# Performance work log

Hardware: AMD Instinct MI355X
Metric: run time of the kernel (lower is better)

## Reference

```python
import jax, jax.numpy as jnp
import numpy as np

N_NODES = 50000
BN_EPS = 1e-5


def gcn_conv(x, W, b, src, dst):
    # PyG GCNConv: linear, add self-loops, symmetric degree normalization, scatter-add, bias.
    h = x @ W                                        # [N, D]
    n = x.shape[0]
    deg = jax.ops.segment_sum(jnp.ones(src.shape[0], x.dtype), dst,
                              num_segments=n) + 1.0  # +1 for self-loop
    dinv = jnp.where(deg > 0, jax.lax.rsqrt(deg), 0.0)
    norm = dinv[src] * dinv[dst]                     # [E]
    agg = jax.ops.segment_sum(h[src] * norm[:, None], dst, num_segments=n)
    agg = agg + h * (dinv * dinv)[:, None]           # self-loop contribution
    return agg + b


def batch_norm(x, gamma, beta):
    # training-mode BN over the node axis (biased variance, as torch)
    mu = jnp.mean(x, axis=0)
    var = jnp.mean((x - mu) ** 2, axis=0)
    return (x - mu) * jax.lax.rsqrt(var + BN_EPS) * gamma + beta


def setup_inputs() -> dict:
    key = jax.random.key(0)
    ks = jax.random.split(key, 8)
    D, C = 128, 10
    x = jax.random.normal(ks[0], (N_NODES, D), dtype=jnp.float32)
    edge_index = jax.random.randint(ks[1], (2, 640000), 0, N_NODES, dtype=jnp.int32)
    s = 1.0 / np.sqrt(D)
    return {
        "x": x,
        "edge_index": edge_index,
        "W1": jax.random.normal(ks[2], (D, D), dtype=jnp.float32) * s,
        "b1": jnp.zeros((D,), jnp.float32),
        "gamma1": jnp.ones((D,), jnp.float32),
        "beta1": jnp.zeros((D,), jnp.float32),
        "W2": jax.random.normal(ks[3], (D, D), dtype=jnp.float32) * s,
        "b2": jnp.zeros((D,), jnp.float32),
        "gamma2": jnp.ones((D,), jnp.float32),
        "beta2": jnp.zeros((D,), jnp.float32),
        "lin1_w": jax.random.normal(ks[4], (D, D), dtype=jnp.float32) * s,
        "lin1_b": jnp.zeros((D,), jnp.float32),
        "lin2_w": jax.random.normal(ks[5], (D, C), dtype=jnp.float32) * s,
        "lin2_b": jnp.zeros((C,), jnp.float32),
    }


def reference(x, edge_index, W1, b1, gamma1, beta1, W2, b2, gamma2, beta2,
              lin1_w, lin1_b, lin2_w, lin2_b):
    src, dst = edge_index[0], edge_index[1]
    # layer 1: GCNConv -> ReLU -> BN (dropout = identity at eval)
    h = jax.nn.relu(gcn_conv(x, W1, b1, src, dst))
    h = batch_norm(h, gamma1, beta1)
    # layer 2
    h = jax.nn.relu(gcn_conv(h, W2, b2, src, dst))
    h = batch_norm(h, gamma2, beta2)
    # MLP head
    h = jax.nn.relu(h @ lin1_w + lin1_b)
    logits = h @ lin2_w + lin2_b
    return jax.nn.log_softmax(logits, axis=-1)
```

## Files before the change

### kernel.cpp

```cpp
#include <hip/hip_runtime.h>
#include <hip/hip_bf16.h>
#include <math.h>

typedef unsigned int uint;
typedef unsigned short ushort;
using f32x4 = __attribute__((ext_vector_type(4))) float;
using s16x8 = __attribute__((ext_vector_type(8))) short;

#define NSLOT 64

__device__ __forceinline__ float bflo(uint u) { return __uint_as_float(u << 16); }
__device__ __forceinline__ float bfhi(uint u) { return __uint_as_float(u & 0xffff0000u); }
__device__ __forceinline__ ushort f2bf(float f) {
    uint u = __float_as_uint(f);
    return (ushort)((u + 0x7fffu + ((u >> 16) & 1u)) >> 16);
}
__device__ __forceinline__ float sel4f(float a, float b, float c, float d, int i) {
    float r = a; r = (i == 1) ? b : r; r = (i == 2) ? c : r; r = (i == 3) ? d : r; return r;
}
__device__ __forceinline__ int sel4i(int a, int b, int c, int d, int i) {
    int r = a; r = (i == 1) ? b : r; r = (i == 2) ? c : r; r = (i == 3) ? d : r; return r;
}


__global__ void deg_count(const int* __restrict__ dst, int* __restrict__ deg, int E) {
    int e = blockIdx.x * 256 + threadIdx.x;
    if (e < E) atomicAdd(&deg[dst[e]], 1);
}

__global__ __launch_bounds__(256) void deg_block_sum(const int* __restrict__ deg,
                                                     int* __restrict__ bsum, int N) {
    __shared__ int s[256];
    int i = blockIdx.x * 256 + threadIdx.x;
    s[threadIdx.x] = (i < N) ? deg[i] : 0;
    __syncthreads();
    #pragma unroll
    for (int off = 128; off > 0; off >>= 1) {
        if (threadIdx.x < off) s[threadIdx.x] += s[threadIdx.x + off];
        __syncthreads();
    }
    if (threadIdx.x == 0) bsum[blockIdx.x] = s[0];
}

__global__ __launch_bounds__(256) void fill_rowstart(const int* __restrict__ deg,
                                                     const int* __restrict__ bsum,
                                                     int* __restrict__ row_start,
                                                     int* __restrict__ cursor,
                                                     float* __restrict__ dinv,
                                                     int N, int E, int nblk) {
    __shared__ int s[256];
    __shared__ int sb[256];
    int t = threadIdx.x;
    int i = blockIdx.x * 256 + t;
    int dg = (i < N) ? deg[i] : 0;
    s[t] = dg;
    sb[t] = (t < nblk) ? bsum[t] : 0;
    __syncthreads();
    for (int off = 1; off < 256; off <<= 1) {
        int v1 = (t >= off) ? s[t - off] : 0;
        int v2 = (t >= off) ? sb[t - off] : 0;
        __syncthreads();
        s[t] += v1;
        sb[t] += v2;
        __syncthreads();
    }
    if (i < N) {
        int boff = (blockIdx.x == 0) ? 0 : sb[blockIdx.x - 1];
        int excl = boff + s[t] - dg;
        row_start[i] = excl;
        cursor[i] = excl;
        dinv[i] = rsqrtf((float)dg + 1.0f);
    }
    if (i == 0) row_start[N] = E;
}

__global__ void csr_fill(const int* __restrict__ src, const int* __restrict__ dst,
                         const float* __restrict__ dinv, int* __restrict__ cursor,
                         int2* __restrict__ csr2, int E) {
    int e = blockIdx.x * 256 + threadIdx.x;
    if (e >= E) return;
    int s = src[e], d = dst[e];
    int pos = atomicAdd(&cursor[d], 1);
    csr2[pos] = make_int2(s, __float_as_int(dinv[s] * dinv[d]));
}


__global__ __launch_bounds__(256) void prep_weights(const float* __restrict__ W1,
                                                    const float* __restrict__ W2,
                                                    const float* __restrict__ W3,
                                                    const float* __restrict__ l2w,
                                                    const float* __restrict__ l2b,
                                                    ushort* __restrict__ wt1,
                                                    ushort* __restrict__ wt2,
                                                    ushort* __restrict__ wt3,
                                                    ushort* __restrict__ w2bf,
                                                    float* __restrict__ b2pad) {
    int i = blockIdx.x * 256 + threadIdx.x;
    int li = i & 16383;
    int k = li >> 7, n = li & 127;
    const float* Ws = (i < 16384) ? W1 : (i < 32768) ? W2 : W3;
    ushort* Wd = (i < 16384) ? wt1 : (i < 32768) ? wt2 : wt3;
    Wd[n * 128 + k] = f2bf(Ws[li]);
    if (i < 2048) {
        int c = i >> 7, kk = i & 127;
        float v = (c < 10) ? l2w[kk * 10 + c] : 0.f;
        w2bf[c * 128 + kk] = f2bf(v);
    }
    if (i < 16) b2pad[i] = (i < 10) ? l2b[i] : -1e30f;
}


template<bool XF32, bool AFF, bool BIAS, bool RELU, bool HEAD>
__global__ __launch_bounds__(256) void gemm_mfma(const void* __restrict__ Xv,
                                                 const float* __restrict__ scale,
                                                 const float* __restrict__ shift,
                                                 const ushort* __restrict__ Bt,
                                                 const float* __restrict__ bias,
                                                 ushort* __restrict__ Y,
                                                 const ushort* __restrict__ W2bf,
                                                 const float* __restrict__ b2pad,
                                                 float* __restrict__ OUT, int N) {
    __shared__ char smem[16384 + 32768];
    char* Al = smem;
    char* Bl = smem + 16384;

    int tid = threadIdx.x;
    int brow = blockIdx.x * 64;

    {
        int n = tid >> 1, h = tid & 1;
        const uint4* srcp = (const uint4*)(Bt + n * 128 + h * 64);
        #pragma unroll
        for (int i = 0; i < 8; ++i) {
            uint4 v = srcp[i];
            int u = (h * 8 + i) ^ (n & 7);
            *(uint4*)(Bl + n * 256 + u * 16) = v;
        }
    }
    {
        int r = tid >> 2, c0 = (tid & 3) * 32;
        int row = brow + r;
        bool ok = row < N;
        uint pk[16];
        if (XF32) {
            const float* Xr = (const float*)Xv + (size_t)row * 128 + c0;
            #pragma unroll
            for (int i = 0; i < 16; ++i) {
                float f0 = ok ? Xr[i * 2] : 0.f;
                float f1 = ok ? Xr[i * 2 + 1] : 0.f;
                pk[i] = (uint)f2bf(f0) | ((uint)f2bf(f1) << 16);
            }
        } else {
            const uint* Xr = (const uint*)((const ushort*)Xv + (size_t)row * 128 + c0);
            #pragma unroll
            for (int i = 0; i < 16; ++i) {
                uint u = ok ? Xr[i] : 0u;
                float f0 = bflo(u), f1 = bfhi(u);
                if (AFF) {
                    int c = c0 + i * 2;
                    f0 = f0 * scale[c] + shift[c];
                    f1 = f1 * scale[c + 1] + shift[c + 1];
                }
                pk[i] = (uint)f2bf(f0) | ((uint)f2bf(f1) << 16);
            }
        }
        #pragma unroll
        for (int i = 0; i < 4; ++i) {
            int u = ((tid & 3) * 4 + i) ^ (r & 7);
            *(uint4*)(Al + r * 256 + u * 16) = *(uint4*)&pk[i * 4];
        }
    }
    __syncthreads();

    int lane = tid & 63, w = tid >> 6;
    int m = lane & 15, g = lane >> 4;
    int wr = w * 16;

    f32x4 acc[8];
    #pragma unroll
    for (int nt = 0; nt < 8; ++nt) acc[nt] = (f32x4){0.f, 0.f, 0.f, 0.f};

    #pragma unroll
    for (int kk = 0; kk < 4; ++kk) {
        int u = (kk * 4 + g) ^ (m & 7);
        s16x8 a = *(const s16x8*)(Al + (wr + m) * 256 + u * 16);
        #pragma unroll
        for (int nt = 0; nt < 8; ++nt) {
            s16x8 b = *(const s16x8*)(Bl + (nt * 16 + m) * 256 + u * 16);
            acc[nt] = __builtin_amdgcn_mfma_f32_16x16x32_bf16(a, b, acc[nt], 0, 0, 0);
        }
    }

    float bv[8];
    if (BIAS) {
        #pragma unroll
        for (int nt = 0; nt < 8; ++nt) bv[nt] = bias[nt * 16 + m];
    }

    if (!HEAD) {
        #pragma unroll
        for (int i = 0; i < 4; ++i) {
            int row = brow + wr + g * 4 + i;
            if (row < N) {
                #pragma unroll
                for (int nt = 0; nt < 8; ++nt) {
                    float v = acc[nt][i];
                    if (BIAS) v += bv[nt];
                    if (RELU) v = fmaxf(v, 0.f);
                    Y[(size_t)row * 128 + nt * 16 + m] = f2bf(v);
                }
            }
        }
    } else {
        #pragma unroll
        for (int i = 0; i < 4; ++i) {
            int r = wr + g * 4 + i;
            #pragma unroll
            for (int nt = 0; nt < 8; ++nt) {
                float v = acc[nt][i] + bv[nt];
                v = fmaxf(v, 0.f);
                int col = nt * 16 + m;
                int u = (col >> 3) ^ (r & 7);
                *(ushort*)(Al + r * 256 + u * 16 + (col & 7) * 2) = f2bf(v);
            }
        }
        __syncthreads();
        float b2v = b2pad[m];
        f32x4 lg = (f32x4){b2v, b2v, b2v, b2v};
        #pragma unroll
        for (int kk = 0; kk < 4; ++kk) {
            int u = (kk * 4 + g) ^ (m & 7);
            s16x8 a = *(const s16x8*)(Al + (wr + m) * 256 + u * 16);
            s16x8 b = *(const s16x8*)(&W2bf[m * 128 + (kk * 4 + g) * 8]);
            lg = __builtin_amdgcn_mfma_f32_16x16x32_bf16(a, b, lg, 0, 0, 0);
        }
        #pragma unroll
        for (int i = 0; i < 4; ++i) {
            float v = lg[i];
            float mx = v;
            #pragma unroll
            for (int off = 8; off > 0; off >>= 1) mx = fmaxf(mx, __shfl_xor(mx, off, 64));
            float ex = expf(v - mx);
            float sm = ex;
            #pragma unroll
            for (int off = 8; off > 0; off >>= 1) sm += __shfl_xor(sm, off, 64);
            float res = v - (mx + logf(sm));
            int grow = brow + wr + g * 4 + i;
            if (m < 10 && grow < N) OUT[(size_t)grow * 10 + m] = res;
        }
    }
}


__global__ __launch_bounds__(256) void gather_fused(const ushort* __restrict__ H,
                                                    const int* __restrict__ row_start,
                                                    const int2* __restrict__ csr2,
                                                    const float* __restrict__ dinv,
                                                    const float* __restrict__ bias,
                                                    ushort* __restrict__ Y,
                                                    float* __restrict__ bnpart, int N) {
    int g = threadIdx.x >> 6, lane = threadIdx.x & 63;
    int d = lane * 2;
    float b0 = bias[d], b1 = bias[d + 1];
    float s0 = 0.f, s1 = 0.f, ss0 = 0.f, ss1 = 0.f;

    int nchunks = (N + 3) / 4;
    int chunk = blockIdx.x * 4 + g;

    if (chunk < nchunks) {
        int c = chunk * 4;
        int nn = min(4, N - c);

        int rsv = row_start[c + min(lane, nn)];
        int rs0 = __shfl(rsv, 0);
        int rs1 = __shfl(rsv, min(1, nn));
        int rs2 = __shfl(rsv, min(2, nn));
        int rs3 = __shfl(rsv, min(3, nn));
        int rs4 = __shfl(rsv, nn);

        float dvv = dinv[c + min(lane, nn - 1)];
        float dv0 = __shfl(dvv, 0);
        float dv1 = __shfl(dvv, min(1, nn - 1));
        float dv2 = __shfl(dvv, min(2, nn - 1));
        float dv3 = __shfl(dvv, min(3, nn - 1));

        uint h0 = *(const uint*)&H[(size_t)c * 128 + d];
        uint h1 = (nn > 1) ? *(const uint*)&H[(size_t)(c + 1) * 128 + d] : 0u;
        uint h2 = (nn > 2) ? *(const uint*)&H[(size_t)(c + 2) * 128 + d] : 0u;
        uint h3 = (nn > 3) ? *(const uint*)&H[(size_t)(c + 3) * 128 + d] : 0u;

        float i0_0 = bflo(h0) * dv0 * dv0 + b0, i1_0 = bfhi(h0) * dv0 * dv0 + b1;
        float i0_1 = bflo(h1) * dv1 * dv1 + b0, i1_1 = bfhi(h1) * dv1 * dv1 + b1;
        float i0_2 = bflo(h2) * dv2 * dv2 + b0, i1_2 = bfhi(h2) * dv2 * dv2 + b1;
        float i0_3 = bflo(h3) * dv3 * dv3 + b0, i1_3 = bfhi(h3) * dv3 * dv3 + b1;

        int e0 = rs0, eend = rs4;
        int seg = 0;
        int nextb = rs1;
        float a0 = i0_0, a1 = i1_0;

        for (int base = e0; base < eend; base += 64) {
            int cnt = min(64, eend - base);
            int2 me = (lane < cnt) ? csr2[base + lane] : make_int2(0, 0);
            int sl = me.x;
            float nl = __int_as_float(me.y);

            for (int j = 0; j < cnt; j += 16) {
                int mm = min(16, cnt - j);
                uint v[16]; float nr[16];
                #pragma unroll
                for (int k = 0; k < 16; ++k) {
                    int idx = min(j + k, cnt - 1);
                    int sk = __shfl(sl, idx);
                    float nk = __shfl(nl, idx);
                    nr[k] = (k < mm) ? nk : 0.f;
                    v[k] = *(const uint*)&H[(size_t)sk * 128 + d];
                }
                #pragma unroll
                for (int k = 0; k < 16; ++k) {
                    if (k < mm) {
                        int e = base + j + k;
                        while (e >= nextb) {
                            float r0 = fmaxf(a0, 0.f), r1 = fmaxf(a1, 0.f);
                            *(uint*)&Y[(size_t)(c + seg) * 128 + d] =
                                (uint)f2bf(r0) | ((uint)f2bf(r1) << 16);
                            s0 += r0; ss0 += r0 * r0; s1 += r1; ss1 += r1 * r1;
                            seg++;
                            a0 = sel4f(i0_0, i0_1, i0_2, i0_3, seg);
                            a1 = sel4f(i1_0, i1_1, i1_2, i1_3, seg);
                            nextb = sel4i(rs1, rs2, rs3, rs4, seg);
                        }
                        a0 += bflo(v[k]) * nr[k];
                        a1 += bfhi(v[k]) * nr[k];
                    }
                }
            }
        }
        for (;;) {
            float r0 = fmaxf(a0, 0.f), r1 = fmaxf(a1, 0.f);
            *(uint*)&Y[(size_t)(c + seg) * 128 + d] = (uint)f2bf(r0) | ((uint)f2bf(r1) << 16);
            s0 += r0; ss0 += r0 * r0; s1 += r1; ss1 += r1 * r1;
            seg++;
            if (seg >= nn) break;
            a0 = sel4f(i0_0, i0_1, i0_2, i0_3, seg);
            a1 = sel4f(i1_0, i1_1, i1_2, i1_3, seg);
            nextb = sel4i(rs1, rs2, rs3, rs4, seg);
        }
    }

    float* bp = bnpart + (size_t)(blockIdx.x & (NSLOT - 1)) * 256;
    __shared__ float red[4][128];
    red[g][d] = s0; red[g][d + 1] = s1;
    __syncthreads();
    if (g == 0) {
        atomicAdd(&bp[d],     red[0][d] + red[1][d] + red[2][d] + red[3][d]);
        atomicAdd(&bp[d + 1], red[0][d + 1] + red[1][d + 1] + red[2][d + 1] + red[3][d + 1]);
    }
    __syncthreads();
    red[g][d] = ss0; red[g][d + 1] = ss1;
    __syncthreads();
    if (g == 0) {
        atomicAdd(&bp[128 + d],     red[0][d] + red[1][d] + red[2][d] + red[3][d]);
        atomicAdd(&bp[128 + d + 1], red[0][d + 1] + red[1][d + 1] + red[2][d + 1] + red[3][d + 1]);
    }
}

__global__ void bnfinalize(float* __restrict__ bnpart,
                           const float* __restrict__ gamma, const float* __restrict__ beta,
                           float* __restrict__ scale, float* __restrict__ shift, float invN) {
    int d = threadIdx.x;
    float sum = 0.f, ss = 0.f;
    #pragma unroll 8
    for (int s = 0; s < NSLOT; ++s) {
        sum += bnpart[s * 256 + d];
        ss  += bnpart[s * 256 + 128 + d];
        bnpart[s * 256 + d] = 0.f;
        bnpart[s * 256 + 128 + d] = 0.f;
    }
    float mu  = sum * invN;
    float var = ss * invN - mu * mu;
    float sc  = gamma[d] * rsqrtf(var + 1e-5f);
    scale[d] = sc;
    shift[d] = beta[d] - mu * sc;
}


static inline char* align16(char* p) { return (char*)(((uintptr_t)p + 15) & ~(uintptr_t)15); }

extern "C" void kernel_launch(void* const* d_in, const int* in_sizes, int n_in,
                              void* d_out, int out_size, void* d_ws, size_t ws_size,
                              hipStream_t stream) {
    const float* x    = (const float*)d_in[0];
    const int*   ei   = (const int*)d_in[1];
    const float* W1   = (const float*)d_in[2];
    const float* b1   = (const float*)d_in[3];
    const float* g1   = (const float*)d_in[4];
    const float* be1  = (const float*)d_in[5];
    const float* W2   = (const float*)d_in[6];
    const float* b2   = (const float*)d_in[7];
    const float* g2   = (const float*)d_in[8];
    const float* be2  = (const float*)d_in[9];
    const float* l1w  = (const float*)d_in[10];
    const float* l1b  = (const float*)d_in[11];
    const float* l2w  = (const float*)d_in[12];
    const float* l2b  = (const float*)d_in[13];
    float* out = (float*)d_out;

    int N = in_sizes[0] / 128;
    int E = in_sizes[1] / 2;
    const int* srcp = ei;
    const int* dstp = ei + E;

    char* w = (char*)d_ws;
    ushort* bufA  = (ushort*)w;  w = align16(w + (size_t)N * 128 * 2);
    ushort* bufB  = (ushort*)w;  w = align16(w + (size_t)N * 128 * 2);
    int*   degc   = (int*)w;     w += (size_t)N * 4;
    float* bnpart = (float*)w;   w = align16(w + (size_t)NSLOT * 256 * 4);
    float* dinv   = (float*)w;   w = align16(w + (size_t)N * 4);
    int*   row_st = (int*)w;     w = align16(w + (size_t)(N + 1) * 4);
    int*   cursor = (int*)w;     w = align16(w + (size_t)N * 4);
    int*   bsum   = (int*)w;     w = align16(w + 256 * 4);
    int2*  csr2   = (int2*)w;    w = align16(w + (size_t)E * 8);
    float* scale  = (float*)w;   w = align16(w + 128 * 4);
    float* shift  = (float*)w;   w = align16(w + 128 * 4);
    ushort* wt1   = (ushort*)w;  w = align16(w + 16384 * 2);
    ushort* wt2   = (ushort*)w;  w = align16(w + 16384 * 2);
    ushort* wt3   = (ushort*)w;  w = align16(w + 16384 * 2);
    ushort* w2bf  = (ushort*)w;  w = align16(w + 2048 * 2);
    float* b2pad  = (float*)w;   w = align16(w + 16 * 4);

    int eg = (E + 255) / 256;
    int ng = (N + 255) / 256;
    int gemm_grid = (N + 63) / 64;
    int nchunks = (N + 3) / 4;
    int gather_grid = (nchunks + 3) / 4;

    hipMemsetAsync(degc, 0, ((size_t)N + NSLOT * 256) * 4, stream);
    deg_count<<<eg, 256, 0, stream>>>(dstp, degc, E);
    deg_block_sum<<<ng, 256, 0, stream>>>(degc, bsum, N);
    fill_rowstart<<<ng, 256, 0, stream>>>(degc, bsum, row_st, cursor, dinv, N, E, ng);
    csr_fill<<<eg, 256, 0, stream>>>(srcp, dstp, dinv, cursor, csr2, E);
    prep_weights<<<192, 256, 0, stream>>>(W1, W2, l1w, l2w, l2b, wt1, wt2, wt3, w2bf, b2pad);

    gemm_mfma<true, false, false, false, false><<<gemm_grid, 256, 0, stream>>>(
        x, nullptr, nullptr, wt1, nullptr, bufA, nullptr, nullptr, nullptr, N);
    gather_fused<<<gather_grid, 256, 0, stream>>>(bufA, row_st, csr2, dinv, b1, bufB, bnpart, N);
    bnfinalize<<<1, 128, 0, stream>>>(bnpart, g1, be1, scale, shift, 1.0f / N);

    gemm_mfma<false, true, false, false, false><<<gemm_grid, 256, 0, stream>>>(
        bufB, scale, shift, wt2, nullptr, bufA, nullptr, nullptr, nullptr, N);
    gather_fused<<<gather_grid, 256, 0, stream>>>(bufA, row_st, csr2, dinv, b2, bufB, bnpart, N);
    bnfinalize<<<1, 128, 0, stream>>>(bnpart, g2, be2, scale, shift, 1.0f / N);

    gemm_mfma<false, true, true, true, true><<<gemm_grid, 256, 0, stream>>>(
        bufB, scale, shift, wt3, l1b, nullptr, w2bf, b2pad, out, N);
}
```

Measured before the change: 329.5 us.

## Factor GCN normalization into GEMM prescale and drop per-edge weights from CSR

The GEMM epilogue now multiplies each output row by dinv[row], so the gather only sums neighbor features and scales by the destination dinv. This lets the CSR store only source indices (4 bytes per edge instead of 8), cutting gather index traffic and per-edge multiplies. The GEMM also processes two 64-row tiles per block to reuse the staged weight tile, and the degree-count and CSR-fill kernels handle two edges per thread. Rounding the prescaled features to bf16 changes numerics slightly, and the doubled shared memory may reduce occupancy.

After: 323.3 us. About the same (-1.9%).

```diff
diff --git a/kernel.cpp b/kernel.cpp
--- a/kernel.cpp
+++ b/kernel.cpp
@@ -24,8 +24,15 @@
 
 
 __global__ void deg_count(const int* __restrict__ dst, int* __restrict__ deg, int E) {
-    int e = blockIdx.x * 256 + threadIdx.x;
-    if (e < E) atomicAdd(&deg[dst[e]], 1);
+    int e0 = blockIdx.x * 512 + threadIdx.x;
+    int e1 = e0 + 256;
+    if (e1 < E) {
+        int dA = dst[e0], dB = dst[e1];
+        atomicAdd(&deg[dA], 1);
+        atomicAdd(&deg[dB], 1);
+    } else if (e0 < E) {
+        atomicAdd(&deg[dst[e0]], 1);
+    }
 }
 
 __global__ __launch_bounds__(256) void deg_block_sum(const int* __restrict__ deg,
@@ -75,13 +82,21 @@
 }
 
 __global__ void csr_fill(const int* __restrict__ src, const int* __restrict__ dst,
-                         const float* __restrict__ dinv, int* __restrict__ cursor,
-                         int2* __restrict__ csr2, int E) {
-    int e = blockIdx.x * 256 + threadIdx.x;
-    if (e >= E) return;
-    int s = src[e], d = dst[e];
-    int pos = atomicAdd(&cursor[d], 1);
-    csr2[pos] = make_int2(s, __float_as_int(dinv[s] * dinv[d]));
+                         int* __restrict__ cursor, int* __restrict__ csr_src, int E) {
+    int e0 = blockIdx.x * 512 + threadIdx.x;
+    int e1 = e0 + 256;
+    if (e1 < E) {
+        int sA = src[e0], dA = dst[e0];
+        int sB = src[e1], dB = dst[e1];
+        int pA = atomicAdd(&cursor[dA], 1);
+        int pB = atomicAdd(&cursor[dB], 1);
+        csr_src[pA] = sA;
+        csr_src[pB] = sB;
+    } else if (e0 < E) {
+        int s = src[e0], d = dst[e0];
+        int p = atomicAdd(&cursor[d], 1);
+        csr_src[p] = s;
+    }
 }
 
 
@@ -110,22 +125,22 @@
 }
 
 
-template<bool XF32, bool AFF, bool BIAS, bool RELU, bool HEAD>
+template<bool XF32, bool AFF, bool PRESCALE, bool HEAD>
 __global__ __launch_bounds__(256) void gemm_mfma(const void* __restrict__ Xv,
                                                  const float* __restrict__ scale,
                                                  const float* __restrict__ shift,
                                                  const ushort* __restrict__ Bt,
                                                  const float* __restrict__ bias,
+                                                 const float* __restrict__ dinv,
                                                  ushort* __restrict__ Y,
                                                  const ushort* __restrict__ W2bf,
                                                  const float* __restrict__ b2pad,
                                                  float* __restrict__ OUT, int N) {
-    __shared__ char smem[16384 + 32768];
-    char* Al = smem;
-    char* Bl = smem + 16384;
+    __shared__ char smem[2 * 16384 + 32768];
+    char* Bl = smem + 32768;
 
     int tid = threadIdx.x;
-    int brow = blockIdx.x * 64;
+    int brow = blockIdx.x * 128;
 
     {
         int n = tid >> 1, h = tid & 1;
@@ -137,116 +152,119 @@
             *(uint4*)(Bl + n * 256 + u * 16) = v;
         }
     }
-    {
-        int r = tid >> 2, c0 = (tid & 3) * 32;
-        int row = brow + r;
-        bool ok = row < N;
-        uint pk[16];
-        if (XF32) {
-            const float* Xr = (const float*)Xv + (size_t)row * 128 + c0;
-            #pragma unroll
-            for (int i = 0; i < 16; ++i) {
-                float f0 = ok ? Xr[i * 2] : 0.f;
-                float f1 = ok ? Xr[i * 2 + 1] : 0.f;
-                pk[i] = (uint)f2bf(f0) | ((uint)f2bf(f1) << 16);
-            }
-        } else {
-            const uint* Xr = (const uint*)((const ushort*)Xv + (size_t)row * 128 + c0);
-            #pragma unroll
-            for (int i = 0; i < 16; ++i) {
-                uint u = ok ? Xr[i] : 0u;
-                float f0 = bflo(u), f1 = bfhi(u);
-                if (AFF) {
-                    int c = c0 + i * 2;
-                    f0 = f0 * scale[c] + shift[c];
-                    f1 = f1 * scale[c + 1] + shift[c + 1];
-                }
-                pk[i] = (uint)f2bf(f0) | ((uint)f2bf(f1) << 16);
-            }
-        }
-        #pragma unroll
-        for (int i = 0; i < 4; ++i) {
-            int u = ((tid & 3) * 4 + i) ^ (r & 7);
-            *(uint4*)(Al + r * 256 + u * 16) = *(uint4*)&pk[i * 4];
-        }
-    }
-    __syncthreads();
 
     int lane = tid & 63, w = tid >> 6;
     int m = lane & 15, g = lane >> 4;
     int wr = w * 16;
 
-    f32x4 acc[8];
     #pragma unroll
-    for (int nt = 0; nt < 8; ++nt) acc[nt] = (f32x4){0.f, 0.f, 0.f, 0.f};
-
-    #pragma unroll
-    for (int kk = 0; kk < 4; ++kk) {
-        int u = (kk * 4 + g) ^ (m & 7);
-        s16x8 a = *(const s16x8*)(Al + (wr + m) * 256 + u * 16);
+    for (int t = 0; t < 2; ++t) {
+        char* Al = smem + t * 16384;
+        int rbase = brow + t * 64;
+
+        {
+            int r = tid >> 2, c0 = (tid & 3) * 32;
+            int row = rbase + r;
+            bool ok = row < N;
+            uint pk[16];
+            if (XF32) {
+                const float* Xr = (const float*)Xv + (size_t)row * 128 + c0;
+                #pragma unroll
+                for (int i = 0; i < 16; ++i) {
+                    float f0 = ok ? Xr[i * 2] : 0.f;
+                    float f1 = ok ? Xr[i * 2 + 1] : 0.f;
+                    pk[i] = (uint)f2bf(f0) | ((uint)f2bf(f1) << 16);
+                }
+            } else {
+                const uint* Xr = (const uint*)((const ushort*)Xv + (size_t)row * 128 + c0);
+                #pragma unroll
+                for (int i = 0; i < 16; ++i) {
+                    uint u = ok ? Xr[i] : 0u;
+                    float f0 = bflo(u), f1 = bfhi(u);
+                    if (AFF) {
+                        int c = c0 + i * 2;
+                        f0 = f0 * scale[c] + shift[c];
+                        f1 = f1 * scale[c + 1] + shift[c + 1];
+                    }
+                    pk[i] = (uint)f2bf(f0) | ((uint)f2bf(f1) << 16);
+                }
+            }
+            #pragma unroll
+            for (int i = 0; i < 4; ++i) {
+                int u = ((tid & 3) * 4 + i) ^ (r & 7);
+                *(uint4*)(Al + r * 256 + u * 16) = *(uint4*)&pk[i * 4];
+            }
+        }
+        __syncthreads();
+
+        f32x4 acc[8];
         #pragma unroll
-        for (int nt = 0; nt < 8; ++nt) {
-            s16x8 b = *(const s16x8*)(Bl + (nt * 16 + m) * 256 + u * 16);
-            acc[nt] = __builtin_amdgcn_mfma_f32_16x16x32_bf16(a, b, acc[nt], 0, 0, 0);
-        }
-    }
-
-    float bv[8];
-    if (BIAS) {
-        #pragma unroll
-        for (int nt = 0; nt < 8; ++nt) bv[nt] = bias[nt * 16 + m];
-    }
-
-    if (!HEAD) {
-        #pragma unroll
-        for (int i = 0; i < 4; ++i) {
-            int row = brow + wr + g * 4 + i;
-            if (row < N) {
-                #pragma unroll
-                for (int nt = 0; nt < 8; ++nt) {
-                    float v = acc[nt][i];
-                    if (BIAS) v += bv[nt];
-                    if (RELU) v = fmaxf(v, 0.f);
-                    Y[(size_t)row * 128 + nt * 16 + m] = f2bf(v);
-                }
-            }
-        }
-    } else {
-        #pragma unroll
-        for (int i = 0; i < 4; ++i) {
-            int r = wr + g * 4 + i;
-            #pragma unroll
-            for (int nt = 0; nt < 8; ++nt) {
-                float v = acc[nt][i] + bv[nt];
-                v = fmaxf(v, 0.f);
-                int col = nt * 16 + m;
-                int u = (col >> 3) ^ (r & 7);
-                *(ushort*)(Al + r * 256 + u * 16 + (col & 7) * 2) = f2bf(v);
-            }
-        }
-        __syncthreads();
-        float b2v = b2pad[m];
-        f32x4 lg = (f32x4){b2v, b2v, b2v, b2v};
+        for (int nt = 0; nt < 8; ++nt) acc[nt] = (f32x4){0.f, 0.f, 0.f, 0.f};
+
         #pragma unroll
         for (int kk = 0; kk < 4; ++kk) {
             int u = (kk * 4 + g) ^ (m & 7);
             s16x8 a = *(const s16x8*)(Al + (wr + m) * 256 + u * 16);
-            s16x8 b = *(const s16x8*)(&W2bf[m * 128 + (kk * 4 + g) * 8]);
-            lg = __builtin_amdgcn_mfma_f32_16x16x32_bf16(a, b, lg, 0, 0, 0);
-        }
-        #pragma unroll
-        for (int i = 0; i < 4; ++i) {
-            float v = lg[i];
-            float mx = v;
-            #pragma unroll
-            for (int off = 8; off > 0; off >>= 1) mx = fmaxf(mx, __shfl_xor(mx, off, 64));
-            float ex = expf(v - mx);
-            float sm = ex;
-            #pragma unroll
-            for (int off = 8; off > 0; off >>= 1) sm += __shfl_xor(sm, off, 64);
-            float res = v - (mx + logf(sm));
-            int grow = brow + wr + g * 4 + i;
-            if (m < 10 && grow < N) OUT[(size_t)grow * 10 + m] = res;
+            #pragma unroll
+            for (int nt = 0; nt < 8; ++nt) {
+                s16x8 b = *(const s16x8*)(Bl + (nt * 16 + m) * 256 + u * 16);
+                acc[nt] = __builtin_amdgcn_mfma_f32_16x16x32_bf16(a, b, acc[nt], 0, 0, 0);
+            }
+        }
+
+        if (!HEAD) {
+            #pragma unroll
+            for (int i = 0; i < 4; ++i) {
+                int row = rbase + wr + g * 4 + i;
+                if (row < N) {
+                    float dv = PRESCALE ? dinv[row] : 1.f;
+                    #pragma unroll
+                    for (int nt = 0; nt < 8; ++nt) {
+                        float v = acc[nt][i];
+                        if (PRESCALE) v *= dv;
+                        Y[(size_t)row * 128 + nt * 16 + m] = f2bf(v);
+                    }
+                }
+            }
+        } else {
+            float bv[8];
+            #pragma unroll
+            for (int nt = 0; nt < 8; ++nt) bv[nt] = bias[nt * 16 + m];
+            #pragma unroll
+            for (int i = 0; i < 4; ++i) {
+                int r = wr + g * 4 + i;
+                #pragma unroll
+                for (int nt = 0; nt < 8; ++nt) {
+                    float v = fmaxf(acc[nt][i] + bv[nt], 0.f);
+                    int col = nt * 16 + m;
+                    int u = (col >> 3) ^ (r & 7);
+                    *(ushort*)(Al + r * 256 + u * 16 + (col & 7) * 2) = f2bf(v);
+                }
+            }
+            __syncthreads();
+            float b2v = b2pad[m];
+            f32x4 lg = (f32x4){b2v, b2v, b2v, b2v};
+            #pragma unroll
+            for (int kk = 0; kk < 4; ++kk) {
+                int u = (kk * 4 + g) ^ (m & 7);
+                s16x8 a = *(const s16x8*)(Al + (wr + m) * 256 + u * 16);
+                s16x8 b = *(const s16x8*)(&W2bf[m * 128 + (kk * 4 + g) * 8]);
+                lg = __builtin_amdgcn_mfma_f32_16x16x32_bf16(a, b, lg, 0, 0, 0);
+            }
+            #pragma unroll
+            for (int i = 0; i < 4; ++i) {
+                float v = lg[i];
+                float mx = v;
+                #pragma unroll
+                for (int off = 8; off > 0; off >>= 1) mx = fmaxf(mx, __shfl_xor(mx, off, 64));
+                float ex = expf(v - mx);
+                float sm = ex;
+                #pragma unroll
+                for (int off = 8; off > 0; off >>= 1) sm += __shfl_xor(sm, off, 64);
+                float res = v - (mx + logf(sm));
+                int grow = rbase + wr + g * 4 + i;
+                if (m < 10 && grow < N) OUT[(size_t)grow * 10 + m] = res;
+            }
         }
     }
 }
@@ -254,7 +272,7 @@
 
 __global__ __launch_bounds__(256) void gather_fused(const ushort* __restrict__ H,
                                                     const int* __restrict__ row_start,
-                                                    const int2* __restrict__ csr2,
+                                                    const int* __restrict__ csr_src,
                                                     const float* __restrict__ dinv,
                                                     const float* __restrict__ bias,
                                                     ushort* __restrict__ Y,
@@ -289,31 +307,28 @@
         uint h2 = (nn > 2) ? *(const uint*)&H[(size_t)(c + 2) * 128 + d] : 0u;
         uint h3 = (nn > 3) ? *(const uint*)&H[(size_t)(c + 3) * 128 + d] : 0u;
 
-        float i0_0 = bflo(h0) * dv0 * dv0 + b0, i1_0 = bfhi(h0) * dv0 * dv0 + b1;
-        float i0_1 = bflo(h1) * dv1 * dv1 + b0, i1_1 = bfhi(h1) * dv1 * dv1 + b1;
-        float i0_2 = bflo(h2) * dv2 * dv2 + b0, i1_2 = bfhi(h2) * dv2 * dv2 + b1;
-        float i0_3 = bflo(h3) * dv3 * dv3 + b0, i1_3 = bfhi(h3) * dv3 * dv3 + b1;
+        float i0_0 = bflo(h0) * dv0 + b0, i1_0 = bfhi(h0) * dv0 + b1;
+        float i0_1 = bflo(h1) * dv1 + b0, i1_1 = bfhi(h1) * dv1 + b1;
+        float i0_2 = bflo(h2) * dv2 + b0, i1_2 = bfhi(h2) * dv2 + b1;
+        float i0_3 = bflo(h3) * dv3 + b0, i1_3 = bfhi(h3) * dv3 + b1;
 
         int e0 = rs0, eend = rs4;
         int seg = 0;
         int nextb = rs1;
-        float a0 = i0_0, a1 = i1_0;
+        float i0s = i0_0, i1s = i1_0, dvs = dv0;
+        float es0 = 0.f, es1 = 0.f;
 
         for (int base = e0; base < eend; base += 64) {
             int cnt = min(64, eend - base);
-            int2 me = (lane < cnt) ? csr2[base + lane] : make_int2(0, 0);
-            int sl = me.x;
-            float nl = __int_as_float(me.y);
+            int sl = (lane < cnt) ? csr_src[base + lane] : 0;
 
             for (int j = 0; j < cnt; j += 16) {
                 int mm = min(16, cnt - j);
-                uint v[16]; float nr[16];
+                uint v[16];
                 #pragma unroll
                 for (int k = 0; k < 16; ++k) {
                     int idx = min(j + k, cnt - 1);
                     int sk = __shfl(sl, idx);
-                    float nk = __shfl(nl, idx);
-                    nr[k] = (k < mm) ? nk : 0.f;
                     v[k] = *(const uint*)&H[(size_t)sk * 128 + d];
                 }
                 #pragma unroll
@@ -321,30 +336,36 @@
                     if (k < mm) {
                         int e = base + j + k;
                         while (e >= nextb) {
-                            float r0 = fmaxf(a0, 0.f), r1 = fmaxf(a1, 0.f);
+                            float r0 = fmaxf(es0 * dvs + i0s, 0.f);
+                            float r1 = fmaxf(es1 * dvs + i1s, 0.f);
                             *(uint*)&Y[(size_t)(c + seg) * 128 + d] =
                                 (uint)f2bf(r0) | ((uint)f2bf(r1) << 16);
                             s0 += r0; ss0 += r0 * r0; s1 += r1; ss1 += r1 * r1;
                             seg++;
-                            a0 = sel4f(i0_0, i0_1, i0_2, i0_3, seg);
-                            a1 = sel4f(i1_0, i1_1, i1_2, i1_3, seg);
+                            i0s = sel4f(i0_0, i0_1, i0_2, i0_3, seg);
+                            i1s = sel4f(i1_0, i1_1, i1_2, i1_3, seg);
+                            dvs = sel4f(dv0, dv1, dv2, dv3, seg);
                             nextb = sel4i(rs1, rs2, rs3, rs4, seg);
+                            es0 = 0.f; es1 = 0.f;
                         }
-                        a0 += bflo(v[k]) * nr[k];
-                        a1 += bfhi(v[k]) * nr[k];
+                        es0 += bflo(v[k]);
+                        es1 += bfhi(v[k]);
                     }
                 }
             }
         }
         for (;;) {
-            float r0 = fmaxf(a0, 0.f), r1 = fmaxf(a1, 0.f);
+            float r0 = fmaxf(es0 * dvs + i0s, 0.f);
+            float r1 = fmaxf(es1 * dvs + i1s, 0.f);
             *(uint*)&Y[(size_t)(c + seg) * 128 + d] = (uint)f2bf(r0) | ((uint)f2bf(r1) << 16);
             s0 += r0; ss0 += r0 * r0; s1 += r1; ss1 += r1 * r1;
             seg++;
             if (seg >= nn) break;
-            a0 = sel4f(i0_0, i0_1, i0_2, i0_3, seg);
-            a1 = sel4f(i1_0, i1_1, i1_2, i1_3, seg);
+            i0s = sel4f(i0_0, i0_1, i0_2, i0_3, seg);
+            i1s = sel4f(i1_0, i1_1, i1_2, i1_3, seg);
+            dvs = sel4f(dv0, dv1, dv2, dv3, seg);
             nextb = sel4i(rs1, rs2, rs3, rs4, seg);
+            es0 = 0.f; es1 = 0.f;
         }
     }
 
@@ -412,46 +433,46 @@
     const int* dstp = ei + E;
 
     char* w = (char*)d_ws;
-    ushort* bufA  = (ushort*)w;  w = align16(w + (size_t)N * 128 * 2);
-    ushort* bufB  = (ushort*)w;  w = align16(w + (size_t)N * 128 * 2);
-    int*   degc   = (int*)w;     w += (size_t)N * 4;
-    float* bnpart = (float*)w;   w = align16(w + (size_t)NSLOT * 256 * 4);
-    float* dinv   = (float*)w;   w = align16(w + (size_t)N * 4);
-    int*   row_st = (int*)w;     w = align16(w + (size_t)(N + 1) * 4);
-    int*   cursor = (int*)w;     w = align16(w + (size_t)N * 4);
-    int*   bsum   = (int*)w;     w = align16(w + 256 * 4);
-    int2*  csr2   = (int2*)w;    w = align16(w + (size_t)E * 8);
-    float* scale  = (float*)w;   w = align16(w + 128 * 4);
-    float* shift  = (float*)w;   w = align16(w + 128 * 4);
-    ushort* wt1   = (ushort*)w;  w = align16(w + 16384 * 2);
-    ushort* wt2   = (ushort*)w;  w = align16(w + 16384 * 2);
-    ushort* wt3   = (ushort*)w;  w = align16(w + 16384 * 2);
-    ushort* w2bf  = (ushort*)w;  w = align16(w + 2048 * 2);
-    float* b2pad  = (float*)w;   w = align16(w + 16 * 4);
-
-    int eg = (E + 255) / 256;
+    ushort* bufA   = (ushort*)w;  w = align16(w + (size_t)N * 128 * 2);
+    ushort* bufB   = (ushort*)w;  w = align16(w + (size_t)N * 128 * 2);
+    int*   degc    = (int*)w;     w += (size_t)N * 4;
+    float* bnpart  = (float*)w;   w = align16(w + (size_t)NSLOT * 256 * 4);
+    float* dinv    = (float*)w;   w = align16(w + (size_t)N * 4);
+    int*   row_st  = (int*)w;     w = align16(w + (size_t)(N + 1) * 4);
+    int*   cursor  = (int*)w;     w = align16(w + (size_t)N * 4);
+    int*   bsum    = (int*)w;     w = align16(w + 256 * 4);
+    int*   csr_src = (int*)w;     w = align16(w + (size_t)E * 4);
+    float* scale   = (float*)w;   w = align16(w + 128 * 4);
+    float* shift   = (float*)w;   w = align16(w + 128 * 4);
+    ushort* wt1    = (ushort*)w;  w = align16(w + 16384 * 2);
+    ushort* wt2    = (ushort*)w;  w = align16(w + 16384 * 2);
+    ushort* wt3    = (ushort*)w;  w = align16(w + 16384 * 2);
+    ushort* w2bf   = (ushort*)w;  w = align16(w + 2048 * 2);
+    float* b2pad   = (float*)w;   w = align16(w + 16 * 4);
+
+    int eg2 = (E + 511) / 512;
     int ng = (N + 255) / 256;
-    int gemm_grid = (N + 63) / 64;
+    int gemm_grid = (N + 127) / 128;
     int nchunks = (N + 3) / 4;
     int gather_grid = (nchunks + 3) / 4;
 
     hipMemsetAsync(degc, 0, ((size_t)N + NSLOT * 256) * 4, stream);
-    deg_count<<<eg, 256, 0, stream>>>(dstp, degc, E);
+    deg_count<<<eg2, 256, 0, stream>>>(dstp, degc, E);
     deg_block_sum<<<ng, 256, 0, stream>>>(degc, bsum, N);
     fill_rowstart<<<ng, 256, 0, stream>>>(degc, bsum, row_st, cursor, dinv, N, E, ng);
-    csr_fill<<<eg, 256, 0, stream>>>(srcp, dstp, dinv, cursor, csr2, E);
+    csr_fill<<<eg2, 256, 0, stream>>>(srcp, dstp, cursor, csr_src, E);
     prep_weights<<<192, 256, 0, stream>>>(W1, W2, l1w, l2w, l2b, wt1, wt2, wt3, w2bf, b2pad);
 
-    gemm_mfma<true, false, false, false, false><<<gemm_grid, 256, 0, stream>>>(
-        x, nullptr, nullptr, wt1, nullptr, bufA, nullptr, nullptr, nullptr, N);
-    gather_fused<<<gather_grid, 256, 0, stream>>>(bufA, row_st, csr2, dinv, b1, bufB, bnpart, N);
+    gemm_mfma<true, false, true, false><<<gemm_grid, 256, 0, stream>>>(
+        x, nullptr, nullptr, wt1, nullptr, dinv, bufA, nullptr, nullptr, nullptr, N);
+    gather_fused<<<gather_grid, 256, 0, stream>>>(bufA, row_st, csr_src, dinv, b1, bufB, bnpart, N);
     bnfinalize<<<1, 128, 0, stream>>>(bnpart, g1, be1, scale, shift, 1.0f / N);
 
-    gemm_mfma<false, true, false, false, false><<<gemm_grid, 256, 0, stream>>>(
-        bufB, scale, shift, wt2, nullptr, bufA, nullptr, nullptr, nullptr, N);
-    gather_fused<<<gather_grid, 256, 0, stream>>>(bufA, row_st, csr2, dinv, b2, bufB, bnpart, N);
+    gemm_mfma<false, true, true, false><<<gemm_grid, 256, 0, stream>>>(
+        bufB, scale, shift, wt2, nullptr, dinv, bufA, nullptr, nullptr, nullptr, N);
+    gather_fused<<<gather_grid, 256, 0, stream>>>(bufA, row_st, csr_src, dinv, b2, bufB, bnpart, N);
     bnfinalize<<<1, 128, 0, stream>>>(bnpart, g2, be2, scale, shift, 1.0f / N);
 
-    gemm_mfma<false, true, true, true, true><<<gemm_grid, 256, 0, stream>>>(
-        bufB, scale, shift, wt3, l1b, nullptr, w2bf, b2pad, out, N);
-}
+    gemm_mfma<false, true, false, true><<<gemm_grid, 256, 0, stream>>>(
+        bufB, scale, shift, wt3, l1b, nullptr, nullptr, w2bf, b2pad, out, N);
+}
```
